# Kernel tuning notes

Measured on AMD Instinct MI355X. Metric: run time of the kernel, lower is better.

Reference implementation:

```python
import jax, jax.numpy as jnp
import numpy as np

EPS = 1e-5

def _layernorm(x, w, b):
    mu = jnp.mean(x, axis=-1, keepdims=True)
    var = jnp.var(x, axis=-1, keepdims=True)
    return (x - mu) * jax.lax.rsqrt(var + EPS) * w + b

def setup_inputs() -> dict:
    key = jax.random.key(0)
    ks = jax.random.split(key, 9)
    b, s, dim = 4, 4096, 2048
    m, n, dim_ctx = 8, 64, 1024
    heads, dim_head = 8, 64
    inner = heads * dim_head
    x = jax.random.normal(ks[0], (b, s, dim), dtype=jnp.float32)
    context = jax.random.normal(ks[1], (b, m, n, dim_ctx), dtype=jnp.float32)
    media_locations = jax.random.randint(ks[2], (b, s), 0, m, dtype=jnp.int64)
    scale = 0.02
    norm_w = jnp.ones((dim,), jnp.float32)
    norm_b = jnp.zeros((dim,), jnp.float32)
    normc_w = jnp.ones((dim_ctx,), jnp.float32)
    normc_b = jnp.zeros((dim_ctx,), jnp.float32)
    Wq = jax.random.normal(ks[3], (dim, inner), jnp.float32) * scale
    Wkv = jax.random.normal(ks[4], (dim_ctx, 2 * inner), jnp.float32) * scale
    Wout = jax.random.normal(ks[5], (inner, dim), jnp.float32) * scale
    return {"x": x, "context": context, "media_locations": media_locations,
            "norm_w": norm_w, "norm_b": norm_b, "normc_w": normc_w, "normc_b": normc_b,
            "Wq": Wq, "Wkv": Wkv, "Wout": Wout}

def reference(x, context, media_locations, norm_w, norm_b, normc_w, normc_b, Wq, Wkv, Wout):
    heads, dim_head = 8, 64
    b, m, n, dc = context.shape
    scale = dim_head ** -0.5
    xn = _layernorm(x, norm_w, norm_b)                       # [b,s,dim]
    ctx = _layernorm(context.reshape(b, m * n, dc), normc_w, normc_b)  # [b,mn,dc]
    q = xn @ Wq                                              # [b,s,inner]
    kv = ctx @ Wkv                                           # [b,mn,2*inner]
    k, v = jnp.split(kv, 2, axis=-1)
    def to_heads(t):
        return t.reshape(t.shape[0], t.shape[1], heads, dim_head).transpose(0, 2, 1, 3)
    q, k, v = to_heads(q), to_heads(k), to_heads(v)          # [b,h,*,d]
    sim = jnp.einsum('bhid,bhjd->bhij', q, k) * scale        # [b,h,s,mn]
    # image-causal mask: kv token j belongs to image j//n; query i may only
    # attend to image media_locations[b,i] (negative index => all masked)
    j_img = jnp.arange(m * n) // n                           # [mn]
    allowed = (media_locations[:, :, None] == j_img[None, None, :]) & (media_locations[:, :, None] >= 0)
    sim = jnp.where(allowed[:, None, :, :], sim, -jnp.inf)
    attn = jax.nn.softmax(sim, axis=-1)
    out = jnp.einsum('bhij,bhjd->bhid', attn, v)             # [b,h,s,d]
    out = out.transpose(0, 2, 1, 3).reshape(b, x.shape[1], heads * dim_head)
    return out @ Wout
```

## Files before the change

### kernel.cpp

```cpp
#include <hip/hip_runtime.h>

typedef unsigned short u16;
typedef unsigned int u32;
typedef __attribute__((ext_vector_type(8))) short short8;
typedef __attribute__((ext_vector_type(4))) short short4_t;
typedef __attribute__((ext_vector_type(4))) float f32x4;

__device__ __forceinline__ float bf2f(u16 u){ return __uint_as_float(((u32)u)<<16); }
__device__ __forceinline__ u16 f2bf(float f){ u32 x = __float_as_uint(f); return (u16)((x + 0x7FFFu + ((x>>16)&1u)) >> 16); }

#define OFF_FLAG   ((size_t)0)
#define OFF_COUNTS ((size_t)256)
#define OFF_LISTS  ((size_t)4096)
#define OFF_XN     ((size_t)(1<<20))
#define OFF_CTXN   (OFF_XN    + (size_t)67108864)
#define OFF_WQT    (OFF_CTXN  + (size_t)4194304)
#define OFF_WKVT   (OFF_WQT   + (size_t)2097152)
#define OFF_WOUTT  (OFF_WKVT  + (size_t)2097152)
#define OFF_Q      (OFF_WOUTT + (size_t)2097152)
#define OFF_KV     (OFF_Q     + (size_t)16777216)
#define OFF_ATTN   (OFF_KV    + (size_t)4194304)
#define OFF_VT     (OFF_ATTN  + (size_t)16777216)
#define WS_NEEDED  (OFF_VT    + (size_t)2097152)

__global__ void prep_kernel(const int* __restrict__ ml32, int* __restrict__ flag, int* __restrict__ counts){
  int t = threadIdx.x;
  if (t < 32) counts[t] = 0;
  __shared__ int nz;
  if (t == 0) nz = 0;
  __syncthreads();
  if (t < 128 && ml32[2*t+1] != 0) atomicAdd(&nz, 1);
  __syncthreads();
  if (t == 0) flag[0] = (nz == 0) ? 1 : 0;
}

template<int D>
__global__ __launch_bounds__(256) void ln_bf16(const float* __restrict__ x, const float* __restrict__ w,
                                               const float* __restrict__ b, u16* __restrict__ out){
  constexpr int VEC = D/256;
  int row = blockIdx.x;
  const float* xr = x + (size_t)row*D;
  int tid = threadIdx.x;
  float v[VEC];
  #pragma unroll
  for (int i=0;i<VEC;i+=4){
    f32x4 f = *(const f32x4*)(xr + tid*VEC + i);
    v[i]=f[0]; v[i+1]=f[1]; v[i+2]=f[2]; v[i+3]=f[3];
  }
  float s=0.f, sq=0.f;
  #pragma unroll
  for (int i=0;i<VEC;++i){ s += v[i]; sq += v[i]*v[i]; }
  #pragma unroll
  for (int off=32;off;off>>=1){ s += __shfl_xor(s,off,64); sq += __shfl_xor(sq,off,64); }
  __shared__ float red[8];
  int lane = tid&63, wid = tid>>6;
  if (lane==0){ red[wid]=s; red[4+wid]=sq; }
  __syncthreads();
  s  = red[0]+red[1]+red[2]+red[3];
  sq = red[4]+red[5]+red[6]+red[7];
  float mu = s/(float)D;
  float var = sq/(float)D - mu*mu;
  float rs = rsqrtf(var + 1e-5f);
  u16 o[VEC];
  #pragma unroll
  for (int i=0;i<VEC;i+=4){
    f32x4 wv = *(const f32x4*)(w + tid*VEC + i);
    f32x4 bv = *(const f32x4*)(b + tid*VEC + i);
    #pragma unroll
    for (int u=0;u<4;++u) o[i+u] = f2bf((v[i+u]-mu)*rs*wv[u] + bv[u]);
  }
  if constexpr (VEC==8) *(short8*)(out + (size_t)row*D + tid*8) = *(short8*)o;
  else                  *(short4_t*)(out + (size_t)row*D + tid*4) = *(short4_t*)o;
}

__global__ __launch_bounds__(256) void transpose_w(const float* __restrict__ in, u16* __restrict__ out, int K, int N){
  __shared__ float t[32][33];
  int tx = threadIdx.x, ty = threadIdx.y;
  int n0 = blockIdx.x*32, k0 = blockIdx.y*32;
  #pragma unroll
  for (int r=0;r<32;r+=8) t[ty+r][tx] = in[(size_t)(k0+ty+r)*N + n0+tx];
  __syncthreads();
  #pragma unroll
  for (int r=0;r<32;r+=8) out[(size_t)(n0+ty+r)*K + k0+tx] = f2bf(t[tx][ty+r]);
}

__global__ __launch_bounds__(256) void transpose_v(const u16* __restrict__ kvb, u16* __restrict__ vt){
  int h = blockIdx.x, bl = blockIdx.y;
  __shared__ u16 t[64][72];
  int tid = threadIdx.x;
  const u16* src = kvb + (size_t)(bl*64)*1024 + 512 + h*64;
  #pragma unroll
  for (int i=0;i<2;++i){
    int idx = i*2048 + tid*8;
    int key = idx>>6, d = idx&63;
    *(short8*)&t[key][d] = *(const short8*)(src + (size_t)key*1024 + d);
  }
  __syncthreads();
  u16* dst = vt + (size_t)(bl*8+h)*4096;
  #pragma unroll
  for (int i=0;i<2;++i){
    int idx = i*2048 + tid*8;
    int d = idx>>6, k0 = idx&63;
    u16 tmp[8];
    #pragma unroll
    for (int u=0;u<8;++u) tmp[u] = t[k0+u][d];
    *(short8*)(dst + d*64 + k0) = *(short8*)tmp;
  }
}

template<int MODE>
__global__ __launch_bounds__(256) void gemm_bt(const u16* __restrict__ A, const u16* __restrict__ B,
                                               void* __restrict__ Cv, int M, int N, int K){
  __shared__ __align__(16) u16 lds[2][2][128*32];
  int tid = threadIdx.x, lane = tid&63, wid = tid>>6;
  int nbn = N>>7;
  int nwg = gridDim.x;
  int wg = blockIdx.x;
  int cpx = nwg>>3;
  wg = (wg&7)*cpx + (wg>>3);
  int brow = wg/nbn, bcol = wg%nbn;

  auto stage = [&](int buf, int kt){
    #pragma unroll
    for (int i=0;i<2;++i){
      int cb = i*256 + wid*64;
      int c  = cb + lane;
      int row = c>>2, kc = c&3;
      const u16* ga = A + (size_t)(brow*128+row)*K + kt*32 + kc*8;
      __builtin_amdgcn_global_load_lds((const __attribute__((address_space(1))) u32*)ga,
          (__attribute__((address_space(3))) u32*)&lds[buf][0][cb*8], 16, 0, 0);
      const u16* gb = B + (size_t)(bcol*128+row)*K + kt*32 + kc*8;
      __builtin_amdgcn_global_load_lds((const __attribute__((address_space(1))) u32*)gb,
          (__attribute__((address_space(3))) u32*)&lds[buf][1][cb*8], 16, 0, 0);
    }
  };

  int wm = wid>>1, wn = wid&1;
  f32x4 acc[4][4] = {};
  int nkt = K>>5;
  stage(0,0);
  __syncthreads();
  for (int kt=0; kt<nkt; ++kt){
    int cur = kt&1;
    if (kt+1<nkt) stage(cur^1, kt+1);
    short8 af[4], bfr[4];
    int r = lane&15, kq = lane>>4;
    #pragma unroll
    for (int mi=0;mi<4;++mi) af[mi]  = *(const short8*)&lds[cur][0][(wm*64+mi*16+r)*32 + kq*8];
    #pragma unroll
    for (int ni=0;ni<4;++ni) bfr[ni] = *(const short8*)&lds[cur][1][(wn*64+ni*16+r)*32 + kq*8];
    #pragma unroll
    for (int mi=0;mi<4;++mi)
      #pragma unroll
      for (int ni=0;ni<4;++ni)
        acc[mi][ni] = __builtin_amdgcn_mfma_f32_16x16x32_bf16(af[mi], bfr[ni], acc[mi][ni], 0,0,0);
    __syncthreads();
  }
  int r4 = (lane>>4)*4, cc = lane&15;
  #pragma unroll
  for (int mi=0;mi<4;++mi)
    #pragma unroll
    for (int ni=0;ni<4;++ni)
      #pragma unroll
      for (int rr=0;rr<4;++rr){
        int row = brow*128 + wm*64 + mi*16 + r4 + rr;
        int col = bcol*128 + wn*64 + ni*16 + cc;
        float val = acc[mi][ni][rr];
        if (MODE==2) val *= 0.125f;
        if (MODE)  ((u16*)Cv)[(size_t)row*N+col] = f2bf(val);
        else       ((float*)Cv)[(size_t)row*N+col] = val;
      }
}

__global__ void bucket_kernel(const int* __restrict__ ml32, const int* __restrict__ flag,
                              int* __restrict__ counts, int* __restrict__ lists){
  int i = blockIdx.x*256 + threadIdx.x;
  int loc = flag[0] ? ml32[2*i] : ml32[i];
  int bl = (i>>12)*8 + loc;
  int pos = atomicAdd(&counts[bl], 1);
  lists[bl*4096 + pos] = i & 4095;
}

__global__ __launch_bounds__(512) void attn_mfma2(const u16* __restrict__ qb, const u16* __restrict__ kvb,
                                                  const u16* __restrict__ vt, u16* __restrict__ ob,
                                                  const int* __restrict__ counts, const int* __restrict__ lists){
  int bl = blockIdx.y, chunk = blockIdx.x;
  int cnt = counts[bl];
  int q0 = chunk*32;
  if (q0 >= cnt) return;
  int b = bl>>3, loc = bl&7;
  int tid = threadIdx.x, lane = tid&63, h = tid>>6;
  __shared__ u16 qs[32][520];
  __shared__ u16 plds[8][32][72];
  __shared__ int qi[32];

  if (tid < 32){
    int p = q0 + tid;
    qi[tid] = (p < cnt) ? lists[bl*4096 + p] : -1;
  }
  __syncthreads();

  const u16* qbase = qb + (size_t)(b*4096)*512;
  #pragma unroll
  for (int p=0;p<4;++p){
    int c = p*512 + tid;
    int row = c>>6, cc = c&63;
    int qq = qi[row];
    if (qq >= 0)
      *(short8*)&qs[row][cc*8] = *(const short8*)(qbase + (size_t)qq*512 + cc*8);
  }
  __syncthreads();

  int r = lane&15, g = lane>>4;

  short8 qf[2][2];
  #pragma unroll
  for (int mt=0;mt<2;++mt){
    qf[mt][0] = *(const short8*)&qs[mt*16+r][h*64 + g*8];
    qf[mt][1] = *(const short8*)&qs[mt*16+r][h*64 + 32 + g*8];
  }
  __syncthreads();

  const u16* kbase = kvb + (size_t)(b*512 + loc*64)*1024 + h*64;
  short8 kfr[4][2];
  #pragma unroll
  for (int nt=0;nt<4;++nt){
    const u16* krow = kbase + (size_t)(nt*16 + r)*1024;
    kfr[nt][0] = *(const short8*)(krow + g*8);
    kfr[nt][1] = *(const short8*)(krow + 32 + g*8);
  }

  f32x4 acc[2][4] = {};
  #pragma unroll
  for (int mt=0;mt<2;++mt)
    #pragma unroll
    for (int nt=0;nt<4;++nt){
      acc[mt][nt] = __builtin_amdgcn_mfma_f32_16x16x32_bf16(qf[mt][0], kfr[nt][0], acc[mt][nt], 0,0,0);
      acc[mt][nt] = __builtin_amdgcn_mfma_f32_16x16x32_bf16(qf[mt][1], kfr[nt][1], acc[mt][nt], 0,0,0);
    }

  #pragma unroll
  for (int mt=0;mt<2;++mt){
    #pragma unroll
    for (int rr=0;rr<4;++rr){
      float m = fmaxf(fmaxf(acc[mt][0][rr], acc[mt][1][rr]), fmaxf(acc[mt][2][rr], acc[mt][3][rr]));
      #pragma unroll
      for (int off=1;off<16;off<<=1) m = fmaxf(m, __shfl_xor(m, off));
      float e0 = __expf(acc[mt][0][rr]-m), e1 = __expf(acc[mt][1][rr]-m);
      float e2 = __expf(acc[mt][2][rr]-m), e3 = __expf(acc[mt][3][rr]-m);
      float sum = (e0+e1)+(e2+e3);
      #pragma unroll
      for (int off=1;off<16;off<<=1) sum += __shfl_xor(sum, off);
      float rs = 1.0f/sum;
      int row = mt*16 + g*4 + rr;
      plds[h][row][ 0 + r] = f2bf(e0*rs);
      plds[h][row][16 + r] = f2bf(e1*rs);
      plds[h][row][32 + r] = f2bf(e2*rs);
      plds[h][row][48 + r] = f2bf(e3*rs);
    }
  }

  const u16* vbase = vt + (size_t)(bl*8 + h)*4096;
  short8 vf[2][4];
  #pragma unroll
  for (int nt=0;nt<4;++nt){
    const u16* vrow = vbase + (size_t)(nt*16 + r)*64;
    vf[0][nt] = *(const short8*)(vrow + g*8);
    vf[1][nt] = *(const short8*)(vrow + 32 + g*8);
  }

  f32x4 oacc[2][4] = {};
  #pragma unroll
  for (int mt=0;mt<2;++mt){
    short8 pa0 = *(const short8*)&plds[h][mt*16 + r][g*8];
    short8 pa1 = *(const short8*)&plds[h][mt*16 + r][32 + g*8];
    #pragma unroll
    for (int nt=0;nt<4;++nt){
      oacc[mt][nt] = __builtin_amdgcn_mfma_f32_16x16x32_bf16(pa0, vf[0][nt], oacc[mt][nt], 0,0,0);
      oacc[mt][nt] = __builtin_amdgcn_mfma_f32_16x16x32_bf16(pa1, vf[1][nt], oacc[mt][nt], 0,0,0);
    }
  }

  #pragma unroll
  for (int mt=0;mt<2;++mt)
    #pragma unroll
    for (int rr=0;rr<4;++rr){
      int row = mt*16 + g*4 + rr;
      #pragma unroll
      for (int nt=0;nt<4;++nt)
        qs[row][h*64 + nt*16 + r] = f2bf(oacc[mt][nt][rr]);
    }
  __syncthreads();

  u16* obase = ob + (size_t)(b*4096)*512;
  #pragma unroll
  for (int p=0;p<4;++p){
    int c = p*512 + tid;
    int row = c>>6, cc = c&63;
    int qq = qi[row];
    if (qq >= 0)
      *(short8*)(obase + (size_t)qq*512 + cc*8) = *(const short8*)&qs[row][cc*8];
  }
}

extern "C" void kernel_launch(void* const* d_in, const int* in_sizes, int n_in,
                              void* d_out, int out_size, void* d_ws, size_t ws_size,
                              hipStream_t stream) {
  const float* x    = (const float*)d_in[0];
  const float* ctx  = (const float*)d_in[1];
  const int*   ml   = (const int*)d_in[2];
  const float* nw   = (const float*)d_in[3];
  const float* nb   = (const float*)d_in[4];
  const float* ncw  = (const float*)d_in[5];
  const float* ncb  = (const float*)d_in[6];
  const float* Wq   = (const float*)d_in[7];
  const float* Wkv  = (const float*)d_in[8];
  const float* Wout = (const float*)d_in[9];
  float* out = (float*)d_out;
  char* ws = (char*)d_ws;
  if (ws_size < WS_NEEDED) return;

  int* flag   = (int*)(ws + OFF_FLAG);
  int* counts = (int*)(ws + OFF_COUNTS);
  int* lists  = (int*)(ws + OFF_LISTS);
  u16* xn     = (u16*)(ws + OFF_XN);
  u16* ctxn   = (u16*)(ws + OFF_CTXN);
  u16* WqT    = (u16*)(ws + OFF_WQT);
  u16* WkvT   = (u16*)(ws + OFF_WKVT);
  u16* WoutT  = (u16*)(ws + OFF_WOUTT);
  u16* qbuf   = (u16*)(ws + OFF_Q);
  u16* kvbuf  = (u16*)(ws + OFF_KV);
  u16* attn_o = (u16*)(ws + OFF_ATTN);
  u16* vtbuf  = (u16*)(ws + OFF_VT);

  prep_kernel<<<1,256,0,stream>>>(ml, flag, counts);
  ln_bf16<2048><<<16384,256,0,stream>>>(x,   nw,  nb,  xn);
  ln_bf16<1024><<<2048, 256,0,stream>>>(ctx, ncw, ncb, ctxn);
  transpose_w<<<dim3(16,64), dim3(32,8),0,stream>>>(Wq,   WqT,   2048, 512);
  transpose_w<<<dim3(32,32), dim3(32,8),0,stream>>>(Wkv,  WkvT,  1024, 1024);
  transpose_w<<<dim3(64,16), dim3(32,8),0,stream>>>(Wout, WoutT, 512,  2048);
  gemm_bt<2><<<512, 256,0,stream>>>(xn,   WqT,  qbuf,  16384, 512,  2048);
  gemm_bt<1><<<128, 256,0,stream>>>(ctxn, WkvT, kvbuf, 2048,  1024, 1024);
  transpose_v<<<dim3(8,32),256,0,stream>>>(kvbuf, vtbuf);
  bucket_kernel<<<64,256,0,stream>>>(ml, flag, counts, lists);
  attn_mfma2<<<dim3(128,32),512,0,stream>>>(qbuf, kvbuf, vtbuf, attn_o, counts, lists);
  gemm_bt<0><<<2048,256,0,stream>>>(attn_o, WoutT, out, 16384, 2048, 512);
}
```

Measured before the change: 237.4 us.

## Store Q in bucket-sorted order and unpermute in the output GEMM epilogue

The Q projection GEMM now scatters its rows into a bucket-sorted order using a precomputed position map. Attention can then read and write contiguous row blocks instead of gathering rows through per-query index lists. The Wout GEMM applies the inverse permutation when it writes its rows, and the three weight transposes are merged into one launch. This adds two small counting and placement kernels plus scattered-row epilogue stores in two GEMMs, in exchange for removing indexed gathers in attention.

New measurement: 272.3 us. +14.7%, slower.

```diff
diff --git a/kernel.cpp b/kernel.cpp
--- a/kernel.cpp
+++ b/kernel.cpp
@@ -11,7 +11,10 @@
 
 #define OFF_FLAG   ((size_t)0)
 #define OFF_COUNTS ((size_t)256)
-#define OFF_LISTS  ((size_t)4096)
+#define OFF_POS    ((size_t)4096)
+#define OFF_INV    (OFF_POS + (size_t)65536)
+#define OFF_OFFS   (OFF_INV + (size_t)65536)
+#define OFF_CURS   (OFF_OFFS + (size_t)256)
 #define OFF_XN     ((size_t)(1<<20))
 #define OFF_CTXN   (OFF_XN    + (size_t)67108864)
 #define OFF_WQT    (OFF_CTXN  + (size_t)4194304)
@@ -23,15 +26,47 @@
 #define OFF_VT     (OFF_ATTN  + (size_t)16777216)
 #define WS_NEEDED  (OFF_VT    + (size_t)2097152)
 
-__global__ void prep_kernel(const int* __restrict__ ml32, int* __restrict__ flag, int* __restrict__ counts){
+__global__ void prep_kernel(const int* __restrict__ ml32, int* __restrict__ flag,
+                            int* __restrict__ counts, int* __restrict__ cursor){
   int t = threadIdx.x;
   if (t < 32) counts[t] = 0;
+  if (t >= 32 && t < 64) cursor[t-32] = 0;
   __shared__ int nz;
   if (t == 0) nz = 0;
   __syncthreads();
-  if (t < 128 && ml32[2*t+1] != 0) atomicAdd(&nz, 1);
+  int odd = 0;
+  #pragma unroll
+  for (int k=0;k<8;++k){ int i = t + k*256; if (ml32[2*i+1] != 0) odd = 1; }
+  if (odd) atomicAdd(&nz, 1);
   __syncthreads();
   if (t == 0) flag[0] = (nz == 0) ? 1 : 0;
+}
+
+__global__ void count_kernel(const int* __restrict__ ml32, const int* __restrict__ flag,
+                             int* __restrict__ counts){
+  int i = blockIdx.x*256 + threadIdx.x;
+  int loc = flag[0] ? ml32[2*i] : ml32[i];
+  atomicAdd(&counts[(i>>12)*8 + loc], 1);
+}
+
+__global__ void place_kernel(const int* __restrict__ ml32, const int* __restrict__ flag,
+                             const int* __restrict__ counts, int* __restrict__ cursor,
+                             int* __restrict__ pos, int* __restrict__ inv, int* __restrict__ offsets){
+  __shared__ int offs[32];
+  int tid = threadIdx.x;
+  if (tid == 0){
+    int a = 0;
+    for (int j=0;j<32;++j){ offs[j] = a; a += counts[j]; }
+  }
+  __syncthreads();
+  int i = blockIdx.x*256 + tid;
+  int loc = flag[0] ? ml32[2*i] : ml32[i];
+  int bl = (i>>12)*8 + loc;
+  int rank = atomicAdd(&cursor[bl], 1);
+  int srow = offs[bl] + rank;
+  pos[i] = srow;
+  inv[srow] = i;
+  if (blockIdx.x == 0 && tid < 32) offsets[tid] = offs[tid];
 }
 
 template<int D>
@@ -73,10 +108,17 @@
   else                  *(short4_t*)(out + (size_t)row*D + tid*4) = *(short4_t*)o;
 }
 
-__global__ __launch_bounds__(256) void transpose_w(const float* __restrict__ in, u16* __restrict__ out, int K, int N){
+__global__ __launch_bounds__(256) void transpose_all(const float* __restrict__ Wq, const float* __restrict__ Wkv,
+                                                     const float* __restrict__ Wout, u16* __restrict__ WqT,
+                                                     u16* __restrict__ WkvT, u16* __restrict__ WoutT){
   __shared__ float t[32][33];
-  int tx = threadIdx.x, ty = threadIdx.y;
-  int n0 = blockIdx.x*32, k0 = blockIdx.y*32;
+  int id = blockIdx.x;
+  const float* in; u16* out; int K, N, tile, tx_n;
+  if (id < 1024)      { in=Wq;   out=WqT;   K=2048; N=512;  tile=id;      tx_n=16; }
+  else if (id < 2048) { in=Wkv;  out=WkvT;  K=1024; N=1024; tile=id-1024; tx_n=32; }
+  else                { in=Wout; out=WoutT; K=512;  N=2048; tile=id-2048; tx_n=64; }
+  int n0 = (tile % tx_n)*32, k0 = (tile / tx_n)*32;
+  int tx = threadIdx.x & 31, ty = threadIdx.x >> 5;
   #pragma unroll
   for (int r=0;r<32;r+=8) t[ty+r][tx] = in[(size_t)(k0+ty+r)*N + n0+tx];
   __syncthreads();
@@ -110,7 +152,8 @@
 
 template<int MODE>
 __global__ __launch_bounds__(256) void gemm_bt(const u16* __restrict__ A, const u16* __restrict__ B,
-                                               void* __restrict__ Cv, int M, int N, int K){
+                                               void* __restrict__ Cv, int M, int N, int K,
+                                               const int* __restrict__ perm){
   __shared__ __align__(16) u16 lds[2][2][128*32];
   int tid = threadIdx.x, lane = tid&63, wid = tid>>6;
   int nbn = N>>7;
@@ -158,56 +201,45 @@
   }
   int r4 = (lane>>4)*4, cc = lane&15;
   #pragma unroll
-  for (int mi=0;mi<4;++mi)
-    #pragma unroll
-    for (int ni=0;ni<4;++ni)
+  for (int mi=0;mi<4;++mi){
+    int rowb = brow*128 + wm*64 + mi*16 + r4;
+    int prow[4];
+    #pragma unroll
+    for (int rr=0;rr<4;++rr) prow[rr] = (MODE==1) ? (rowb+rr) : perm[rowb+rr];
+    #pragma unroll
+    for (int ni=0;ni<4;++ni){
+      int col = bcol*128 + wn*64 + ni*16 + cc;
       #pragma unroll
       for (int rr=0;rr<4;++rr){
-        int row = brow*128 + wm*64 + mi*16 + r4 + rr;
-        int col = bcol*128 + wn*64 + ni*16 + cc;
         float val = acc[mi][ni][rr];
         if (MODE==2) val *= 0.125f;
-        if (MODE)  ((u16*)Cv)[(size_t)row*N+col] = f2bf(val);
-        else       ((float*)Cv)[(size_t)row*N+col] = val;
+        if (MODE)  ((u16*)Cv)[(size_t)prow[rr]*N+col] = f2bf(val);
+        else       ((float*)Cv)[(size_t)prow[rr]*N+col] = val;
       }
-}
-
-__global__ void bucket_kernel(const int* __restrict__ ml32, const int* __restrict__ flag,
-                              int* __restrict__ counts, int* __restrict__ lists){
-  int i = blockIdx.x*256 + threadIdx.x;
-  int loc = flag[0] ? ml32[2*i] : ml32[i];
-  int bl = (i>>12)*8 + loc;
-  int pos = atomicAdd(&counts[bl], 1);
-  lists[bl*4096 + pos] = i & 4095;
-}
-
-__global__ __launch_bounds__(512) void attn_mfma2(const u16* __restrict__ qb, const u16* __restrict__ kvb,
+    }
+  }
+}
+
+__global__ __launch_bounds__(512) void attn_mfma3(const u16* __restrict__ qb, const u16* __restrict__ kvb,
                                                   const u16* __restrict__ vt, u16* __restrict__ ob,
-                                                  const int* __restrict__ counts, const int* __restrict__ lists){
+                                                  const int* __restrict__ counts, const int* __restrict__ offsets){
   int bl = blockIdx.y, chunk = blockIdx.x;
   int cnt = counts[bl];
-  int q0 = chunk*32;
-  if (q0 >= cnt) return;
+  if (chunk*32 >= cnt) return;
+  int base_s = offsets[bl] + chunk*32;
+  int nvalid = cnt - chunk*32; if (nvalid > 32) nvalid = 32;
   int b = bl>>3, loc = bl&7;
   int tid = threadIdx.x, lane = tid&63, h = tid>>6;
   __shared__ u16 qs[32][520];
   __shared__ u16 plds[8][32][72];
-  __shared__ int qi[32];
-
-  if (tid < 32){
-    int p = q0 + tid;
-    qi[tid] = (p < cnt) ? lists[bl*4096 + p] : -1;
-  }
-  __syncthreads();
-
-  const u16* qbase = qb + (size_t)(b*4096)*512;
+
+  const u16* qsrc = qb + (size_t)base_s*512;
   #pragma unroll
   for (int p=0;p<4;++p){
     int c = p*512 + tid;
     int row = c>>6, cc = c&63;
-    int qq = qi[row];
-    if (qq >= 0)
-      *(short8*)&qs[row][cc*8] = *(const short8*)(qbase + (size_t)qq*512 + cc*8);
+    if (base_s + row < 16384)
+      *(short8*)&qs[row][cc*8] = *(const short8*)(qsrc + (size_t)row*512 + cc*8);
   }
   __syncthreads();
 
@@ -292,14 +324,13 @@
     }
   __syncthreads();
 
-  u16* obase = ob + (size_t)(b*4096)*512;
+  u16* odst = ob + (size_t)base_s*512;
   #pragma unroll
   for (int p=0;p<4;++p){
     int c = p*512 + tid;
     int row = c>>6, cc = c&63;
-    int qq = qi[row];
-    if (qq >= 0)
-      *(short8*)(obase + (size_t)qq*512 + cc*8) = *(const short8*)&qs[row][cc*8];
+    if (row < nvalid)
+      *(short8*)(odst + (size_t)row*512 + cc*8) = *(const short8*)&qs[row][cc*8];
   }
 }
 
@@ -320,9 +351,12 @@
   char* ws = (char*)d_ws;
   if (ws_size < WS_NEEDED) return;
 
-  int* flag   = (int*)(ws + OFF_FLAG);
-  int* counts = (int*)(ws + OFF_COUNTS);
-  int* lists  = (int*)(ws + OFF_LISTS);
+  int* flag    = (int*)(ws + OFF_FLAG);
+  int* counts  = (int*)(ws + OFF_COUNTS);
+  int* pos     = (int*)(ws + OFF_POS);
+  int* inv     = (int*)(ws + OFF_INV);
+  int* offsets = (int*)(ws + OFF_OFFS);
+  int* cursor  = (int*)(ws + OFF_CURS);
   u16* xn     = (u16*)(ws + OFF_XN);
   u16* ctxn   = (u16*)(ws + OFF_CTXN);
   u16* WqT    = (u16*)(ws + OFF_WQT);
@@ -333,16 +367,15 @@
   u16* attn_o = (u16*)(ws + OFF_ATTN);
   u16* vtbuf  = (u16*)(ws + OFF_VT);
 
-  prep_kernel<<<1,256,0,stream>>>(ml, flag, counts);
+  prep_kernel<<<1,256,0,stream>>>(ml, flag, counts, cursor);
+  count_kernel<<<64,256,0,stream>>>(ml, flag, counts);
+  place_kernel<<<64,256,0,stream>>>(ml, flag, counts, cursor, pos, inv, offsets);
   ln_bf16<2048><<<16384,256,0,stream>>>(x,   nw,  nb,  xn);
   ln_bf16<1024><<<2048, 256,0,stream>>>(ctx, ncw, ncb, ctxn);
-  transpose_w<<<dim3(16,64), dim3(32,8),0,stream>>>(Wq,   WqT,   2048, 512);
-  transpose_w<<<dim3(32,32), dim3(32,8),0,stream>>>(Wkv,  WkvT,  1024, 1024);
-  transpose_w<<<dim3(64,16), dim3(32,8),0,stream>>>(Wout, WoutT, 512,  2048);
-  gemm_bt<2><<<512, 256,0,stream>>>(xn,   WqT,  qbuf,  16384, 512,  2048);
-  gemm_bt<1><<<128, 256,0,stream>>>(ctxn, WkvT, kvbuf, 2048,  1024, 1024);
+  transpose_all<<<3072, 256,0,stream>>>(Wq, Wkv, Wout, WqT, WkvT, WoutT);
+  gemm_bt<2><<<512, 256,0,stream>>>(xn,   WqT,  qbuf,  16384, 512,  2048, pos);
+  gemm_bt<1><<<128, 256,0,stream>>>(ctxn, WkvT, kvbuf, 2048,  1024, 1024, nullptr);
   transpose_v<<<dim3(8,32),256,0,stream>>>(kvbuf, vtbuf);
-  bucket_kernel<<<64,256,0,stream>>>(ml, flag, counts, lists);
-  attn_mfma2<<<dim3(128,32),512,0,stream>>>(qbuf, kvbuf, vtbuf, attn_o, counts, lists);
-  gemm_bt<0><<<2048,256,0,stream>>>(attn_o, WoutT, out, 16384, 2048, 512);
-}
+  attn_mfma3<<<dim3(128,32),512,0,stream>>>(qbuf, kvbuf, vtbuf, attn_o, counts, offsets);
+  gemm_bt<0><<<2048,256,0,stream>>>(attn_o, WoutT, out, 16384, 2048, 512, inv);
+}
```
